# Kernel optimization log

Hardware: AMD Instinct MI355X
Metric: run time of the kernel (lower is better)

## Reference

```python
import jax, jax.numpy as jnp
import numpy as np

B = 16384          # batch
N = 24             # num_features / fields
CARD = 10000       # vocab per feature (all equal)
D = 16             # factor_dim
NI = N * (N - 1) // 2  # 276 pairwise interactions
H1, H2 = 128, 64


def setup_inputs() -> dict:
    key = jax.random.key(0)
    ks = jax.random.split(key, 10)
    x = jax.random.randint(ks[0], (B, N), 0, CARD, dtype=jnp.int32)
    # field-aware embedding table: E[f, id, field, :] is feature f's embedding w.r.t. field
    E = jax.random.normal(ks[1], (N, CARD, N, D), dtype=jnp.float32) * 0.01
    Wlin = jax.random.normal(ks[2], (N, CARD), dtype=jnp.float32) * 0.01
    blin = jnp.zeros((1,), dtype=jnp.float32)
    W1 = jax.random.normal(ks[3], (NI, H1), dtype=jnp.float32) * (1.0 / np.sqrt(NI))
    b1 = jnp.zeros((H1,), dtype=jnp.float32)
    W2 = jax.random.normal(ks[4], (H1, H2), dtype=jnp.float32) * (1.0 / np.sqrt(H1))
    b2 = jnp.zeros((H2,), dtype=jnp.float32)
    W3 = jax.random.normal(ks[5], (H2, 1), dtype=jnp.float32) * (1.0 / np.sqrt(H2))
    b3 = jnp.zeros((1,), dtype=jnp.float32)
    return {"x": x, "E": E, "Wlin": Wlin, "blin": blin,
            "W1": W1, "b1": b1, "W2": W2, "b2": b2, "W3": W3, "b3": b3}


def reference(x, E, Wlin, blin, W1, b1, W2, b2, W3, b3):
    feat_idx = jnp.arange(N)[None, :]              # [1, N]
    # factors[b, i, j, :] = embedding of feature i (value x[b,i]) w.r.t. field j
    factors = E[feat_idx, x]                        # [B, N, N, D]
    # interactions[b, i, j] = <factors[b,i,j], factors[b,j,i]>
    inter = jnp.sum(factors * jnp.swapaxes(factors, 1, 2), axis=-1)  # [B, N, N]
    iu, ju = jnp.triu_indices(N, k=1)
    pairs = inter[:, iu, ju]                        # [B, NI] strict upper triangle, row-major
    # FCN (dropout inactive at inference): relu -> relu -> linear
    h = jax.nn.relu(pairs @ W1 + b1)
    h = jax.nn.relu(h @ W2 + b2)
    nn_out = h @ W3 + b3                            # [B, 1]
    lin_out = jnp.sum(Wlin[feat_idx, x], axis=1, keepdims=True) + blin  # [B, 1]
    return lin_out + nn_out
```

## Files before the change

### kernel.cpp

```cpp
#include <hip/hip_runtime.h>

#define BB    16384
#define NF    24
#define CARDN 10000
#define DD    16
#define NI    276
#define H1N   128
#define H2N   64
#define SB    16
#define RSTR  392
#define PSTR  17
#define HSTR  17

__global__ __launch_bounds__(256) void fanfm_fused_kernel(
    const int* __restrict__ x, const float* __restrict__ E,
    const float* __restrict__ Wlin, const float* __restrict__ blin,
    const float* __restrict__ W1, const float* __restrict__ b1,
    const float* __restrict__ W2, const float* __restrict__ b2,
    const float* __restrict__ W3, const float* __restrict__ b3,
    float* __restrict__ out)
{
    __shared__ float rows_s[NF * RSTR];
    __shared__ float pairsT[NI * PSTR];
    __shared__ int   xs[SB * NF];
    __shared__ float lin_s[SB];

    float* h1T = rows_s;
    float* h2T = rows_s + H1N * HSTR;

    const int tid = threadIdx.x;
    const int b0  = blockIdx.x * SB;

    for (int idx = tid; idx < SB * NF; idx += 256) xs[idx] = x[b0 * NF + idx];
    __syncthreads();

    if (tid < SB) {
        float l = blin[0] + b3[0];
        #pragma unroll
        for (int i = 0; i < NF; ++i) l += Wlin[i * CARDN + xs[tid * NF + i]];
        lin_s[tid] = l;
    }

    int pi0, pj0, pi1 = -1, pj1 = -1;
    {
        int i = 0, rem = tid, cnt = NF - 1;
        while (rem >= cnt) { rem -= cnt; --cnt; ++i; }
        pi0 = i; pj0 = i + 1 + rem;
    }
    if (tid + 256 < NI) {
        int i = 0, rem = tid + 256, cnt = NF - 1;
        while (rem >= cnt) { rem -= cnt; --cnt; ++i; }
        pi1 = i; pj1 = i + 1 + rem;
    }

    for (int s = 0; s < SB; ++s) {
        __syncthreads();
        #pragma unroll
        for (int k = 0; k < 9; ++k) {
            int idx = tid + k * 256;
            int r   = idx / 96;
            int cq  = idx - r * 96;
            const float4 v = *(const float4*)(E +
                ((size_t)r * CARDN + xs[s * NF + r]) * (NF * DD) + cq * 4);
            *(float4*)(rows_s + r * RSTR + cq * 4) = v;
        }
        __syncthreads();
        {
            const float4* a = (const float4*)(rows_s + pi0 * RSTR + pj0 * DD);
            const float4* c = (const float4*)(rows_s + pj0 * RSTR + pi0 * DD);
            float4 a0 = a[0], a1 = a[1], a2 = a[2], a3 = a[3];
            float4 c0 = c[0], c1 = c[1], c2 = c[2], c3 = c[3];
            float d =
                a0.x*c0.x + a0.y*c0.y + a0.z*c0.z + a0.w*c0.w +
                a1.x*c1.x + a1.y*c1.y + a1.z*c1.z + a1.w*c1.w +
                a2.x*c2.x + a2.y*c2.y + a2.z*c2.z + a2.w*c2.w +
                a3.x*c3.x + a3.y*c3.y + a3.z*c3.z + a3.w*c3.w;
            pairsT[tid * PSTR + s] = d;
        }
        if (pi1 >= 0) {
            const float4* a = (const float4*)(rows_s + pi1 * RSTR + pj1 * DD);
            const float4* c = (const float4*)(rows_s + pj1 * RSTR + pi1 * DD);
            float4 a0 = a[0], a1 = a[1], a2 = a[2], a3 = a[3];
            float4 c0 = c[0], c1 = c[1], c2 = c[2], c3 = c[3];
            float d =
                a0.x*c0.x + a0.y*c0.y + a0.z*c0.z + a0.w*c0.w +
                a1.x*c1.x + a1.y*c1.y + a1.z*c1.z + a1.w*c1.w +
                a2.x*c2.x + a2.y*c2.y + a2.z*c2.z + a2.w*c2.w +
                a3.x*c3.x + a3.y*c3.y + a3.z*c3.z + a3.w*c3.w;
            pairsT[(tid + 256) * PSTR + s] = d;
        }
    }
    __syncthreads();

    {
        const int c4 = tid & 31;
        const int sg = tid >> 5;
        float acc[2][4] = {};
        #pragma unroll 4
        for (int p = 0; p < NI; ++p) {
            float4 w = *(const float4*)(W1 + p * H1N + c4 * 4);
            float pr0 = pairsT[p * PSTR + sg * 2 + 0];
            float pr1 = pairsT[p * PSTR + sg * 2 + 1];
            acc[0][0] = fmaf(pr0, w.x, acc[0][0]);
            acc[0][1] = fmaf(pr0, w.y, acc[0][1]);
            acc[0][2] = fmaf(pr0, w.z, acc[0][2]);
            acc[0][3] = fmaf(pr0, w.w, acc[0][3]);
            acc[1][0] = fmaf(pr1, w.x, acc[1][0]);
            acc[1][1] = fmaf(pr1, w.y, acc[1][1]);
            acc[1][2] = fmaf(pr1, w.z, acc[1][2]);
            acc[1][3] = fmaf(pr1, w.w, acc[1][3]);
        }
        float4 bb = *(const float4*)(b1 + c4 * 4);
        #pragma unroll
        for (int si = 0; si < 2; ++si) {
            int s = sg * 2 + si;
            h1T[(c4 * 4 + 0) * HSTR + s] = fmaxf(acc[si][0] + bb.x, 0.f);
            h1T[(c4 * 4 + 1) * HSTR + s] = fmaxf(acc[si][1] + bb.y, 0.f);
            h1T[(c4 * 4 + 2) * HSTR + s] = fmaxf(acc[si][2] + bb.z, 0.f);
            h1T[(c4 * 4 + 3) * HSTR + s] = fmaxf(acc[si][3] + bb.w, 0.f);
        }
    }
    __syncthreads();

    {
        const int c16 = tid & 15;
        const int sg2 = tid >> 4;
        float acc[4] = {};
        #pragma unroll 4
        for (int p = 0; p < H1N; ++p) {
            float4 w = *(const float4*)(W2 + p * H2N + c16 * 4);
            float pr = h1T[p * HSTR + sg2];
            acc[0] = fmaf(pr, w.x, acc[0]);
            acc[1] = fmaf(pr, w.y, acc[1]);
            acc[2] = fmaf(pr, w.z, acc[2]);
            acc[3] = fmaf(pr, w.w, acc[3]);
        }
        float4 bb = *(const float4*)(b2 + c16 * 4);
        h2T[(c16 * 4 + 0) * HSTR + sg2] = fmaxf(acc[0] + bb.x, 0.f);
        h2T[(c16 * 4 + 1) * HSTR + sg2] = fmaxf(acc[1] + bb.y, 0.f);
        h2T[(c16 * 4 + 2) * HSTR + sg2] = fmaxf(acc[2] + bb.z, 0.f);
        h2T[(c16 * 4 + 3) * HSTR + sg2] = fmaxf(acc[3] + bb.w, 0.f);
    }
    __syncthreads();

    {
        const int s  = tid >> 4;
        const int ko = tid & 15;
        float r = 0.f;
        #pragma unroll
        for (int kk = 0; kk < 4; ++kk) {
            int k = ko * 4 + kk;
            r = fmaf(h2T[k * HSTR + s], W3[k], r);
        }
        r += __shfl_xor(r, 1);
        r += __shfl_xor(r, 2);
        r += __shfl_xor(r, 4);
        r += __shfl_xor(r, 8);
        if (ko == 0) out[b0 + s] = r + lin_s[s];
    }
}

extern "C" void kernel_launch(void* const* d_in, const int* in_sizes, int n_in,
                              void* d_out, int out_size, void* d_ws, size_t ws_size,
                              hipStream_t stream) {
    const int*   x    = (const int*)  d_in[0];
    const float* E    = (const float*)d_in[1];
    const float* Wlin = (const float*)d_in[2];
    const float* blin = (const float*)d_in[3];
    const float* W1   = (const float*)d_in[4];
    const float* b1   = (const float*)d_in[5];
    const float* W2   = (const float*)d_in[6];
    const float* b2   = (const float*)d_in[7];
    const float* W3   = (const float*)d_in[8];
    const float* b3   = (const float*)d_in[9];
    float* out = (float*)d_out;

    fanfm_fused_kernel<<<BB / SB, 256, 0, stream>>>(
        x, E, Wlin, blin, W1, b1, W2, b2, W3, b3, out);
}
```

Baseline: 146.9 us.

## Gather embedding slices directly from global memory instead of staging full rows

The old version staged each sample's 24 full embedding rows (24x384 floats) in shared memory with two barriers per sample. The new version has each thread load only the two 16-float slices a pair needs straight from global memory, over all 16x276 (sample, pair) items in a flat loop. Pair indices come from a shared lookup table, and shared memory shrinks, with launch bounds raised to 4 blocks per SM for higher occupancy. Every byte of each row is still read once per sample, but now as scattered 64-byte accesses rather than staged coalesced loads, and the per-sample barriers are gone.

Measured after the change: 133.5 us. -9.1%, faster.

```diff
diff --git a/kernel.cpp b/kernel.cpp
--- a/kernel.cpp
+++ b/kernel.cpp
@@ -8,11 +8,10 @@
 #define H1N   128
 #define H2N   64
 #define SB    16
-#define RSTR  392
 #define PSTR  17
 #define HSTR  17
 
-__global__ __launch_bounds__(256) void fanfm_fused_kernel(
+__global__ __launch_bounds__(256, 4) void fanfm_fused_kernel(
     const int* __restrict__ x, const float* __restrict__ E,
     const float* __restrict__ Wlin, const float* __restrict__ blin,
     const float* __restrict__ W1, const float* __restrict__ b1,
@@ -20,18 +19,25 @@
     const float* __restrict__ W3, const float* __restrict__ b3,
     float* __restrict__ out)
 {
-    __shared__ float rows_s[NF * RSTR];
     __shared__ float pairsT[NI * PSTR];
+    __shared__ float h1T[H1N * HSTR];
     __shared__ int   xs[SB * NF];
     __shared__ float lin_s[SB];
+    __shared__ int   pi_tab[NI];
+    __shared__ int   pj_tab[NI];
 
-    float* h1T = rows_s;
-    float* h2T = rows_s + H1N * HSTR;
+    float* h2T = pairsT;
 
     const int tid = threadIdx.x;
     const int b0  = blockIdx.x * SB;
 
     for (int idx = tid; idx < SB * NF; idx += 256) xs[idx] = x[b0 * NF + idx];
+    for (int idx = tid; idx < NI; idx += 256) {
+        int i = 0, rem = idx, cnt = NF - 1;
+        while (rem >= cnt) { rem -= cnt; --cnt; ++i; }
+        pi_tab[idx] = i;
+        pj_tab[idx] = i + 1 + rem;
+    }
     __syncthreads();
 
     if (tid < SB) {
@@ -41,33 +47,18 @@
         lin_s[tid] = l;
     }
 
-    int pi0, pj0, pi1 = -1, pj1 = -1;
-    {
-        int i = 0, rem = tid, cnt = NF - 1;
-        while (rem >= cnt) { rem -= cnt; --cnt; ++i; }
-        pi0 = i; pj0 = i + 1 + rem;
-    }
-    if (tid + 256 < NI) {
-        int i = 0, rem = tid + 256, cnt = NF - 1;
-        while (rem >= cnt) { rem -= cnt; --cnt; ++i; }
-        pi1 = i; pj1 = i + 1 + rem;
-    }
-
-    for (int s = 0; s < SB; ++s) {
-        __syncthreads();
-        #pragma unroll
-        for (int k = 0; k < 9; ++k) {
-            int idx = tid + k * 256;
-            int r   = idx / 96;
-            int cq  = idx - r * 96;
-            const float4 v = *(const float4*)(E +
-                ((size_t)r * CARDN + xs[s * NF + r]) * (NF * DD) + cq * 4);
-            *(float4*)(rows_s + r * RSTR + cq * 4) = v;
-        }
-        __syncthreads();
-        {
-            const float4* a = (const float4*)(rows_s + pi0 * RSTR + pj0 * DD);
-            const float4* c = (const float4*)(rows_s + pj0 * RSTR + pi0 * DD);
+    #pragma unroll 2
+    for (int k = 0; k < (SB * NI + 255) / 256; ++k) {
+        int idx = tid + k * 256;
+        if (idx < SB * NI) {
+            int s = idx / NI;
+            int p = idx - s * NI;
+            int i = pi_tab[p];
+            int j = pj_tab[p];
+            int xi = xs[s * NF + i];
+            int xj = xs[s * NF + j];
+            const float4* a = (const float4*)(E + ((size_t)i * CARDN + xi) * (NF * DD) + j * DD);
+            const float4* c = (const float4*)(E + ((size_t)j * CARDN + xj) * (NF * DD) + i * DD);
             float4 a0 = a[0], a1 = a[1], a2 = a[2], a3 = a[3];
             float4 c0 = c[0], c1 = c[1], c2 = c[2], c3 = c[3];
             float d =
@@ -75,19 +66,7 @@
                 a1.x*c1.x + a1.y*c1.y + a1.z*c1.z + a1.w*c1.w +
                 a2.x*c2.x + a2.y*c2.y + a2.z*c2.z + a2.w*c2.w +
                 a3.x*c3.x + a3.y*c3.y + a3.z*c3.z + a3.w*c3.w;
-            pairsT[tid * PSTR + s] = d;
-        }
-        if (pi1 >= 0) {
-            const float4* a = (const float4*)(rows_s + pi1 * RSTR + pj1 * DD);
-            const float4* c = (const float4*)(rows_s + pj1 * RSTR + pi1 * DD);
-            float4 a0 = a[0], a1 = a[1], a2 = a[2], a3 = a[3];
-            float4 c0 = c[0], c1 = c[1], c2 = c[2], c3 = c[3];
-            float d =
-                a0.x*c0.x + a0.y*c0.y + a0.z*c0.z + a0.w*c0.w +
-                a1.x*c1.x + a1.y*c1.y + a1.z*c1.z + a1.w*c1.w +
-                a2.x*c2.x + a2.y*c2.y + a2.z*c2.z + a2.w*c2.w +
-                a3.x*c3.x + a3.y*c3.y + a3.z*c3.z + a3.w*c3.w;
-            pairsT[(tid + 256) * PSTR + s] = d;
+            pairsT[p * PSTR + s] = d;
         }
     }
     __syncthreads();
```
